# Kernel tuning notes

Measured on AMD Instinct MI355X. Metric: run time of the kernel, lower is better.

Reference implementation:

```python
import jax, jax.numpy as jnp
import numpy as np

N, D_IN, D_OUT, E = 8192, 2048, 8192, 8


def setup_inputs() -> dict:
    key = jax.random.key(0)
    k1, k2, k3 = jax.random.split(key, 3)
    x = jax.random.normal(k1, (N, D_IN), dtype=jnp.float32)
    # packed weight layout [E, in, out] (pack() pretransposes [E,out,in] -> [E,in,out])
    weight = jax.random.normal(k2, (E, D_IN, D_OUT), dtype=jnp.float32) * (1.0 / np.sqrt(D_IN))
    indices = jax.random.randint(k3, (N,), 0, E, dtype=jnp.int32)
    return {"x": x, "weight": weight, "indices": indices}


def reference(x, weight, indices):
    # gather_mm: out[n] = x[n] @ weight[indices[n]]  -> [N, D_OUT]
    # Avoid materializing weight[indices] ([N, in, out]); instead loop over the
    # small fixed expert count, masking tokens routed to each expert.
    n_experts = weight.shape[0]
    out = jnp.zeros((x.shape[0], weight.shape[-1]), dtype=x.dtype)
    for e in range(n_experts):
        mask = (indices == e)[:, None]
        xe = jnp.where(mask, x, 0)          # zero out tokens not routed to e
        out = out + xe @ weight[e]           # [N, in] @ [in, out]
    return out
```

## Files before the change

### kernel.cpp

```cpp
#include <hip/hip_runtime.h>
#include <hip/hip_bf16.h>
#include <stdint.h>

#define N_TOK 8192
#define D_IN  2048
#define D_OUT 8192
#define NEXP  8
#define KST   32
#define NT2   40
#define NS2   32
#define AIMG  32768
#define X_OFF2 65536
#define X_BYTES2 ((long)NT2 * KST * AIMG)
#define W_OFF2 (X_OFF2 + X_BYTES2)
#define W_BYTES2 ((long)NEXP * NS2 * KST * AIMG)
#define WS_NEED2 ((size_t)(W_OFF2 + W_BYTES2))


typedef float  f32x4  __attribute__((ext_vector_type(4)));
typedef __bf16 bf16x8 __attribute__((ext_vector_type(8)));

__global__ void SwitchLinear_setup_kernel(const int* __restrict__ idx,
                                          int* __restrict__ ws) {
    __shared__ int cnt[NEXP], cur[NEXP];
    int t = threadIdx.x;
    if (t < NEXP) cnt[t] = 0;
    __syncthreads();
    for (int i = t; i < N_TOK; i += 256) atomicAdd(&cnt[idx[i]], 1);
    __syncthreads();
    if (t == 0) {
        int o = 0, nt = 0, nt1 = 0;
        for (int e = 0; e < NEXP; ++e) {
            cur[e] = o;
            int c = cnt[e];
            for (int r = 0; r < c; r += 256) {
                ws[8 + nt]   = e;
                ws[96 + nt]  = o + r;
                ws[192 + nt] = (c - r < 256) ? (c - r) : 256;
                ++nt;
            }
            for (int r = 0; r < c; r += 128) {
                ws[256 + nt1] = e;
                ws[328 + nt1] = o + r;
                ws[400 + nt1] = (c - r < 128) ? (c - r) : 128;
                ++nt1;
            }
            o += c;
        }
        ws[0] = nt;
        ws[4] = nt1;
    }
    __syncthreads();
    for (int i = t; i < N_TOK; i += 256) {
        int p = atomicAdd(&cur[idx[i]], 1);
        ws[512 + p] = i;
    }
}


__global__ __launch_bounds__(256) void SwitchLinear_convx_kernel(
    const float* __restrict__ x, const int* __restrict__ ws,
    char* __restrict__ wsb) {
    const int tile = blockIdx.x, kst = blockIdx.y;
    if (tile >= ws[0]) return;
    const int rs = ws[96 + tile], rows = ws[192 + tile];
    char* img = wsb + X_OFF2 + (long)(tile * KST + kst) * AIMG;
    const int t = threadIdx.x;
#pragma unroll
    for (int i = 0; i < 8; ++i) {
        int u = t + i * 256;
        int R = u >> 3, kc8 = u & 7;
        int rl = rs + (R < rows ? R : rows - 1);
        int token = ws[512 + rl];
        const float* src = x + (long)token * D_IN + kst * 64 + kc8 * 8;
        f32x4 v0 = *(const f32x4*)src;
        f32x4 v1 = *(const f32x4*)(src + 4);
        union { __bf16 hh[8]; uint4 u4; } c;
        c.hh[0] = (__bf16)v0[0]; c.hh[1] = (__bf16)v0[1];
        c.hh[2] = (__bf16)v0[2]; c.hh[3] = (__bf16)v0[3];
        c.hh[4] = (__bf16)v1[0]; c.hh[5] = (__bf16)v1[1];
        c.hh[6] = (__bf16)v1[2]; c.hh[7] = (__bf16)v1[3];
        int slot = (((R & 1) << 2) | (kc8 & 3)) ^ ((R >> 1) & 7);
        *(uint4*)(img + (kc8 >> 2) * 16384 + ((R >> 1) << 7) + (slot << 4)) = c.u4;
    }
}

__global__ __launch_bounds__(256) void SwitchLinear_convw_kernel(
    const float* __restrict__ w, char* __restrict__ wsb) {
    const int img = blockIdx.x;
    const int kst = img & 31, s = (img >> 5) & 63, e = img >> 11;
    const int y = s >> 1, hh = s & 1;
    __shared__ float tl[64 * 129];
    const float* src = w + (long)e * D_IN * D_OUT + (long)(kst * 64) * D_OUT +
                       y * 256 + hh * 128;
    const int t = threadIdx.x;
#pragma unroll
    for (int i = 0; i < 8; ++i) {
        int u = t + i * 256;
        int row = u >> 5, ch = u & 31;
        f32x4 v = *(const f32x4*)(src + (long)row * D_OUT + ch * 4);
        float* d = &tl[row * 129 + ch * 4];
        d[0] = v[0]; d[1] = v[1]; d[2] = v[2]; d[3] = v[3];
    }
    __syncthreads();
    char* dimg = wsb + W_OFF2 + (long)((e * NS2 + y) * KST + kst) * AIMG;
#pragma unroll
    for (int i = 0; i < 4; ++i) {
        int u = t + i * 256;
        int cl = u >> 3, kc8 = u & 7;
        union { __bf16 h8[8]; uint4 u4; } c;
#pragma unroll
        for (int j = 0; j < 8; ++j) c.h8[j] = (__bf16)tl[(kc8 * 8 + j) * 129 + cl];
        int cc = hh * 128 + cl;
        int slot = (((cc & 1) << 2) | (kc8 & 3)) ^ ((cc >> 1) & 7);
        *(uint4*)(dimg + (kc8 >> 2) * 16384 + ((cc >> 1) << 7) + (slot << 4)) = c.u4;
    }
}


__global__ __launch_bounds__(512, 1) void SwitchLinear_gemm_kernel(
    const char* __restrict__ wsb, const int* __restrict__ ws,
    float* __restrict__ out) {
    const int bid = blockIdx.x;
    const int lb  = (bid & 7) * ((NT2 * NS2) / 8) + (bid >> 3);
    const int tx  = lb % NT2;
    const int y   = lb / NT2;
    if (tx >= ws[0]) return;
    const int e = ws[8 + tx], rs = ws[96 + tx], rows = ws[192 + tx];

    __shared__ __align__(16) char lds[2][2][2][16384];
    __shared__ int ord[256];

    const int t = threadIdx.x;
    if (t < 256) ord[t] = ws[512 + rs + (t < rows ? t : 0)];
    __syncthreads();

    const char* aImg = wsb + X_OFF2 + (long)(tx * KST) * AIMG;
    const char* bImg = wsb + W_OFF2 + (long)((e * NS2 + y) * KST) * AIMG;

    const int lane = t & 63;
    const int wid  = t >> 6;
    const int wr = wid >> 2, wc = wid & 3;
    const int lm = lane & 15, lk = lane >> 4;

    f32x4 acc[8][4];
#pragma unroll
    for (int i = 0; i < 8; ++i)
#pragma unroll
        for (int j = 0; j < 4; ++j) acc[i][j] = (f32x4){0.f, 0.f, 0.f, 0.f};

    bf16x8 aa[4], bb[4];

#define STG(op, ks, half, tt)                                                 \
    __builtin_amdgcn_global_load_lds(                                         \
        (const __attribute__((address_space(1))) uint32_t*)(                  \
            ((op) ? bImg : aImg) + (long)(tt) * AIMG + (ks) * 16384 +         \
            (half) * 8192 + t * 16),                                          \
        (__attribute__((address_space(3))) uint32_t*)(                        \
            &lds[(tt) & 1][op][ks][(half) * 8192 + t * 16]),                  \
        16, 0, 0)

#define SWB(r) ((((r) >> 1) << 7) + (((((((r) & 1) << 2)) | lk) ^ (((r) >> 1) & 7)) << 4))

#define LDB(p, ks)                                                            \
    do { _Pragma("unroll")                                                    \
        for (int ni = 0; ni < 4; ++ni) {                                      \
            int cc = wc * 64 + ni * 16 + lm;                                  \
            bb[ni] = *(const bf16x8*)(&lds[p][1][ks][SWB(cc)]);               \
        } } while (0)

#define LDA(p, ks, mh)                                                        \
    do { _Pragma("unroll")                                                    \
        for (int q = 0; q < 4; ++q) {                                         \
            int rr = wr * 128 + (mh) * 64 + q * 16 + lm;                      \
            aa[q] = *(const bf16x8*)(&lds[p][0][ks][SWB(rr)]);                \
        } } while (0)

#define MFMA16(mh)                                                            \
    do { _Pragma("unroll")                                                    \
        for (int q = 0; q < 4; ++q)                                           \
            _Pragma("unroll")                                                 \
            for (int ni = 0; ni < 4; ++ni)                                    \
                acc[(mh) * 4 + q][ni] = __builtin_amdgcn_mfma_f32_16x16x32_bf16( \
                    aa[q], bb[ni], acc[(mh) * 4 + q][ni], 0, 0, 0);           \
    } while (0)

#define PH(p, ks, mh, DOB, ISSUE, POST)                                       \
    do {                                                                      \
        if (DOB) LDB(p, ks);                                                  \
        LDA(p, ks, mh);                                                       \
        ISSUE;                                                                \
        __builtin_amdgcn_s_barrier();                                         \
        asm volatile("s_waitcnt lgkmcnt(0)" ::: "memory");                    \
        __builtin_amdgcn_sched_barrier(0);                                    \
        __builtin_amdgcn_s_setprio(1);                                        \
        MFMA16(mh);                                                           \
        __builtin_amdgcn_s_setprio(0);                                        \
        POST;                                                                 \
        __builtin_amdgcn_s_barrier();                                         \
    } while (0)

    STG(0, 0, 0, 0); STG(0, 0, 1, 0); STG(1, 0, 0, 0); STG(1, 0, 1, 0);
    STG(0, 1, 0, 0); STG(0, 1, 1, 0); STG(1, 1, 0, 0); STG(1, 1, 1, 0);
    asm volatile("s_waitcnt vmcnt(4)" ::: "memory");
    __builtin_amdgcn_s_barrier();

    for (int tt = 0; tt < KST - 1; ++tt) {
        const int p = tt & 1;
        const int nx = tt + 1;
        PH(p, 0, 0, 1, { STG(0, 0, 0, nx); STG(0, 0, 1, nx); }, ((void)0));
        PH(p, 0, 1, 0, { STG(1, 0, 0, nx); STG(1, 0, 1, nx); },
           asm volatile("s_waitcnt vmcnt(4)" ::: "memory"));
        PH(p, 1, 0, 1, { STG(0, 1, 0, nx); STG(0, 1, 1, nx); }, ((void)0));
        PH(p, 1, 1, 0, { STG(1, 1, 0, nx); STG(1, 1, 1, nx); },
           asm volatile("s_waitcnt vmcnt(4)" ::: "memory"));
    }
    {
        const int p = (KST - 1) & 1;
        PH(p, 0, 0, 1, ((void)0), ((void)0));
        PH(p, 0, 1, 0, ((void)0),
           asm volatile("s_waitcnt vmcnt(0)" ::: "memory"));
        PH(p, 1, 0, 1, ((void)0), ((void)0));
        PH(p, 1, 1, 0, ((void)0), ((void)0));
    }

#pragma unroll
    for (int mi = 0; mi < 8; ++mi) {
#pragma unroll
        for (int j = 0; j < 4; ++j) {
            int rl = wr * 128 + mi * 16 + lk * 4 + j;
            if (rl < rows) {
                int token = ord[rl];
                float* po = out + (long)token * D_OUT + y * 256 + wc * 64 + lm;
#pragma unroll
                for (int ni = 0; ni < 4; ++ni) po[ni * 16] = acc[mi][ni][j];
            }
        }
    }
#undef STG
#undef SWB
#undef LDB
#undef LDA
#undef MFMA16
#undef PH
}


__device__ __forceinline__ int fb_a_byte(int r, int kbyte) {
    return r * 128 + (kbyte ^ ((r & 7) << 4));
}
__device__ __forceinline__ int fb_b_byte(int n, int kbyte) {
    int slot = (n ^ (n >> 2)) & 7;
    return n * 128 + (kbyte ^ (slot << 4));
}

__global__ __launch_bounds__(256, 2) void SwitchLinear_gemm_fb_kernel(
    const float* __restrict__ x, const float* __restrict__ w,
    const int* __restrict__ ws, float* __restrict__ out) {
    const int nt = ws[4];
    const int tx = blockIdx.x;
    if (tx >= nt) return;
    const int e    = ws[256 + tx];
    const int rs   = ws[328 + tx];
    const int rows = ws[400 + tx];
    const int col0 = blockIdx.y * 128;

    __shared__ __align__(16) unsigned short As[128 * 64];
    __shared__ __align__(16) unsigned short Bs[128 * 64];
    __shared__ int ord[128];

    const int t = threadIdx.x;
    if (t < 128) {
        int r = (t < rows) ? (rs + t) : rs;
        ord[t] = ws[512 + r];
    }
    __syncthreads();

    const int kq = t & 15;
    const float* pA[8];
    int rowA[8];
#pragma unroll
    for (int i = 0; i < 8; ++i) {
        int r = (t >> 4) + 16 * i;
        rowA[i] = r;
        pA[i] = x + (long)ord[r] * D_IN + kq * 4;
    }
    const float* pB[2];
    int nB[2], kbB[2];
#pragma unroll
    for (int i = 0; i < 2; ++i) {
        int u = t + 256 * i;
        int kgf = u >> 5, q = u & 31;
        kbB[i] = kgf * 4;
        nB[i]  = q * 4;
        pB[i]  = w + (long)e * D_IN * D_OUT + (long)(kgf * 4) * D_OUT + col0 + q * 4;
    }

    const int lane = t & 63;
    const int wid  = t >> 6;
    const int wr = wid >> 1, wc = wid & 1;
    const int lm = lane & 15, lk = lane >> 4;

    f32x4 acc[4][4];
#pragma unroll
    for (int i = 0; i < 4; ++i)
#pragma unroll
        for (int j = 0; j < 4; ++j) acc[i][j] = (f32x4){0.f, 0.f, 0.f, 0.f};

    for (int k0 = 0; k0 < D_IN; k0 += 64) {
#pragma unroll
        for (int i = 0; i < 8; ++i) {
            f32x4 v = *(const f32x4*)(pA[i] + k0);
            union { __bf16 h[4]; uint2 u; } c;
            c.h[0] = (__bf16)v[0]; c.h[1] = (__bf16)v[1];
            c.h[2] = (__bf16)v[2]; c.h[3] = (__bf16)v[3];
            *(uint2*)((char*)As + fb_a_byte(rowA[i], kq * 8)) = c.u;
        }
#pragma unroll
        for (int i = 0; i < 2; ++i) {
            const float* p = pB[i] + (long)k0 * D_OUT;
            f32x4 r0 = *(const f32x4*)(p);
            f32x4 r1 = *(const f32x4*)(p + D_OUT);
            f32x4 r2 = *(const f32x4*)(p + 2 * D_OUT);
            f32x4 r3 = *(const f32x4*)(p + 3 * D_OUT);
#pragma unroll
            for (int j = 0; j < 4; ++j) {
                int n = nB[i] + j;
                union { __bf16 h[4]; uint2 u; } c;
                c.h[0] = (__bf16)r0[j]; c.h[1] = (__bf16)r1[j];
                c.h[2] = (__bf16)r2[j]; c.h[3] = (__bf16)r3[j];
                *(uint2*)((char*)Bs + fb_b_byte(n, kbB[i] * 2)) = c.u;
            }
        }
        __syncthreads();
#pragma unroll
        for (int ks = 0; ks < 2; ++ks) {
            bf16x8 a[4], b[4];
            const int kbyte = ks * 64 + lk * 16;
#pragma unroll
            for (int mi = 0; mi < 4; ++mi) {
                int r = wr * 64 + mi * 16 + lm;
                a[mi] = *(const bf16x8*)((const char*)As + fb_a_byte(r, kbyte));
            }
#pragma unroll
            for (int ni = 0; ni < 4; ++ni) {
                int n = wc * 64 + ni * 16 + lm;
                b[ni] = *(const bf16x8*)((const char*)Bs + fb_b_byte(n, kbyte));
            }
#pragma unroll
            for (int mi = 0; mi < 4; ++mi)
#pragma unroll
                for (int ni = 0; ni < 4; ++ni)
                    acc[mi][ni] = __builtin_amdgcn_mfma_f32_16x16x32_bf16(
                        a[mi], b[ni], acc[mi][ni], 0, 0, 0);
        }
        __syncthreads();
    }
#pragma unroll
    for (int mi = 0; mi < 4; ++mi) {
#pragma unroll
        for (int j = 0; j < 4; ++j) {
            int rl = wr * 64 + mi * 16 + lk * 4 + j;
            if (rl < rows) {
                int token = ord[rl];
                float* po = out + (long)token * D_OUT + col0 + wc * 64 + lm;
#pragma unroll
                for (int ni = 0; ni < 4; ++ni) po[ni * 16] = acc[mi][ni][j];
            }
        }
    }
}

extern "C" void kernel_launch(void* const* d_in, const int* in_sizes, int n_in,
                              void* d_out, int out_size, void* d_ws, size_t ws_size,
                              hipStream_t stream) {
    const float* x   = (const float*)d_in[0];
    const float* w   = (const float*)d_in[1];
    const int*   idx = (const int*)d_in[2];
    float* out = (float*)d_out;
    int*   ws  = (int*)d_ws;
    char*  wsb = (char*)d_ws;

    SwitchLinear_setup_kernel<<<1, 256, 0, stream>>>(idx, ws);
    if (ws_size >= WS_NEED2) {
        SwitchLinear_convx_kernel<<<dim3(NT2, KST), 256, 0, stream>>>(x, ws, wsb);
        SwitchLinear_convw_kernel<<<NEXP * 64 * KST, 256, 0, stream>>>(w, wsb);
        SwitchLinear_gemm_kernel<<<NT2 * NS2, 512, 0, stream>>>(wsb, ws, out);
    } else {
        dim3 grid(72, 64);
        SwitchLinear_gemm_fb_kernel<<<grid, 256, 0, stream>>>(x, w, ws, out);
    }
}
```

Measured before the change: 565.0 us.

## Triple-buffer B tiles to prefetch two stages ahead; keep token ids in registers

Splits the LDS staging into separate A (double-buffered) and B (triple-buffered) arrays so weight tiles are prefetched two K-stages ahead while activation tiles stay one ahead. The main loop now covers all stages with conditional issue and adjusted vmcnt waits. Token indices for the epilogue are loaded into registers up front, which drops the shared ord array and its initial syncthreads. The change uses more LDS (160KB) and extra registers for tok, and the vmcnt accounting with uneven in-flight load counts risks reading a tile before it arrives or stalling longer.

```diff
diff --git a/kernel.cpp b/kernel.cpp
--- a/kernel.cpp
+++ b/kernel.cpp
@@ -128,12 +128,10 @@
     if (tx >= ws[0]) return;
     const int e = ws[8 + tx], rs = ws[96 + tx], rows = ws[192 + tx];
 
-    __shared__ __align__(16) char lds[2][2][2][16384];
-    __shared__ int ord[256];
+    __shared__ __align__(16) char ldsA[2][2][16384];
+    __shared__ __align__(16) char ldsB[3][2][16384];
 
     const int t = threadIdx.x;
-    if (t < 256) ord[t] = ws[512 + rs + (t < rows ? t : 0)];
-    __syncthreads();
 
     const char* aImg = wsb + X_OFF2 + (long)(tx * KST) * AIMG;
     const char* bImg = wsb + W_OFF2 + (long)((e * NS2 + y) * KST) * AIMG;
@@ -143,6 +141,15 @@
     const int wr = wid >> 2, wc = wid & 3;
     const int lm = lane & 15, lk = lane >> 4;
 
+    int tok[8][4];
+#pragma unroll
+    for (int mi = 0; mi < 8; ++mi)
+#pragma unroll
+        for (int j = 0; j < 4; ++j) {
+            int rl = wr * 128 + mi * 16 + lk * 4 + j;
+            tok[mi][j] = ws[512 + rs + (rl < rows ? rl : 0)];
+        }
+
     f32x4 acc[8][4];
 #pragma unroll
     for (int i = 0; i < 8; ++i)
@@ -151,29 +158,36 @@
 
     bf16x8 aa[4], bb[4];
 
-#define STG(op, ks, half, tt)                                                 \
+#define STGA(ks, half, tt)                                                    \
     __builtin_amdgcn_global_load_lds(                                         \
         (const __attribute__((address_space(1))) uint32_t*)(                  \
-            ((op) ? bImg : aImg) + (long)(tt) * AIMG + (ks) * 16384 +         \
-            (half) * 8192 + t * 16),                                          \
+            aImg + (long)(tt) * AIMG + (ks) * 16384 + (half) * 8192 + t * 16),\
         (__attribute__((address_space(3))) uint32_t*)(                        \
-            &lds[(tt) & 1][op][ks][(half) * 8192 + t * 16]),                  \
+            &ldsA[(tt) & 1][ks][(half) * 8192 + t * 16]),                     \
         16, 0, 0)
 
+#define STGB(ks, half, tt)                                                    \
+    __builtin_amdgcn_global_load_lds(                                         \
+        (const __attribute__((address_space(1))) uint32_t*)(                  \
+            bImg + (long)(tt) * AIMG + (ks) * 16384 + (half) * 8192 + t * 16),\
+        (__attribute__((address_space(3))) uint32_t*)(                        \
+            &ldsB[(tt) % 3][ks][(half) * 8192 + t * 16]),                     \
+        16, 0, 0)
+
 #define SWB(r) ((((r) >> 1) << 7) + (((((((r) & 1) << 2)) | lk) ^ (((r) >> 1) & 7)) << 4))
 
-#define LDB(p, ks)                                                            \
+#define LDB(pb, ks)                                                           \
     do { _Pragma("unroll")                                                    \
         for (int ni = 0; ni < 4; ++ni) {                                      \
             int cc = wc * 64 + ni * 16 + lm;                                  \
-            bb[ni] = *(const bf16x8*)(&lds[p][1][ks][SWB(cc)]);               \
+            bb[ni] = *(const bf16x8*)(&ldsB[pb][ks][SWB(cc)]);                \
         } } while (0)
 
-#define LDA(p, ks, mh)                                                        \
+#define LDA(pa, ks, mh)                                                       \
     do { _Pragma("unroll")                                                    \
         for (int q = 0; q < 4; ++q) {                                         \
             int rr = wr * 128 + (mh) * 64 + q * 16 + lm;                      \
-            aa[q] = *(const bf16x8*)(&lds[p][0][ks][SWB(rr)]);                \
+            aa[q] = *(const bf16x8*)(&ldsA[pa][ks][SWB(rr)]);                 \
         } } while (0)
 
 #define MFMA16(mh)                                                            \
@@ -185,43 +199,45 @@
                     aa[q], bb[ni], acc[(mh) * 4 + q][ni], 0, 0, 0);           \
     } while (0)
 
-#define PH(p, ks, mh, DOB, ISSUE, POST)                                       \
+#define PH(BODY_LD, ISSUE, MH, POST)                                          \
     do {                                                                      \
-        if (DOB) LDB(p, ks);                                                  \
-        LDA(p, ks, mh);                                                       \
+        BODY_LD;                                                              \
         ISSUE;                                                                \
         __builtin_amdgcn_s_barrier();                                         \
         asm volatile("s_waitcnt lgkmcnt(0)" ::: "memory");                    \
         __builtin_amdgcn_sched_barrier(0);                                    \
         __builtin_amdgcn_s_setprio(1);                                        \
-        MFMA16(mh);                                                           \
+        MFMA16(MH);                                                           \
         __builtin_amdgcn_s_setprio(0);                                        \
         POST;                                                                 \
         __builtin_amdgcn_s_barrier();                                         \
     } while (0)
 
-    STG(0, 0, 0, 0); STG(0, 0, 1, 0); STG(1, 0, 0, 0); STG(1, 0, 1, 0);
-    STG(0, 1, 0, 0); STG(0, 1, 1, 0); STG(1, 1, 0, 0); STG(1, 1, 1, 0);
+    STGA(0, 0, 0); STGA(0, 1, 0); STGA(1, 0, 0); STGA(1, 1, 0);
+    STGB(0, 0, 0); STGB(0, 1, 0); STGB(1, 0, 0); STGB(1, 1, 0);
+    STGB(0, 0, 1); STGB(0, 1, 1); STGB(1, 0, 1); STGB(1, 1, 1);
     asm volatile("s_waitcnt vmcnt(4)" ::: "memory");
     __builtin_amdgcn_s_barrier();
 
-    for (int tt = 0; tt < KST - 1; ++tt) {
-        const int p = tt & 1;
-        const int nx = tt + 1;
-        PH(p, 0, 0, 1, { STG(0, 0, 0, nx); STG(0, 0, 1, nx); }, ((void)0));
-        PH(p, 0, 1, 0, { STG(1, 0, 0, nx); STG(1, 0, 1, nx); },
-           asm volatile("s_waitcnt vmcnt(4)" ::: "memory"));
-        PH(p, 1, 0, 1, { STG(0, 1, 0, nx); STG(0, 1, 1, nx); }, ((void)0));
-        PH(p, 1, 1, 0, { STG(1, 1, 0, nx); STG(1, 1, 1, nx); },
-           asm volatile("s_waitcnt vmcnt(4)" ::: "memory"));
-    }
-    {
-        const int p = (KST - 1) & 1;
-        PH(p, 0, 0, 1, ((void)0), ((void)0));
-        PH(p, 0, 1, 0, ((void)0),
-           asm volatile("s_waitcnt vmcnt(0)" ::: "memory"));
-        PH(p, 1, 0, 1, ((void)0), ((void)0));
-        PH(p, 1, 1, 0, ((void)0), ((void)0));
+    for (int tt = 0; tt < KST; ++tt) {
+        const int pa = tt & 1;
+        const int pb = tt % 3;
+        const int nxA = tt + 1;
+        const int nxB = tt + 2;
+        const bool iA = nxA < KST;
+        const bool iB = nxB < KST;
+        PH({ LDB(pb, 0); LDA(pa, 0, 0); },
+           { if (iA) { STGA(0, 0, nxA); STGA(0, 1, nxA); } }, 0, ((void)0));
+        PH({ LDA(pa, 0, 1); },
+           { if (iA) { STGA(1, 0, nxA); STGA(1, 1, nxA); } }, 1, ((void)0));
+        PH({ LDB(pb, 1); LDA(pa, 1, 0); },
+           { if (iB) { STGB(0, 0, nxB); STGB(0, 1, nxB); } }, 0, ((void)0));
+        PH({ LDA(pa, 1, 1); },
+           { if (iB) { STGB(1, 0, nxB); STGB(1, 1, nxB); } }, 1,
+           { if (tt < KST - 2)
+                 asm volatile("s_waitcnt vmcnt(4)" ::: "memory");
+             else if (tt == KST - 2)
+                 asm volatile("s_waitcnt vmcnt(0)" ::: "memory"); });
     }
 
 #pragma unroll
@@ -230,14 +246,14 @@
         for (int j = 0; j < 4; ++j) {
             int rl = wr * 128 + mi * 16 + lk * 4 + j;
             if (rl < rows) {
-                int token = ord[rl];
-                float* po = out + (long)token * D_OUT + y * 256 + wc * 64 + lm;
+                float* po = out + (long)tok[mi][j] * D_OUT + y * 256 + wc * 64 + lm;
 #pragma unroll
                 for (int ni = 0; ni < 4; ++ni) po[ni * 16] = acc[mi][ni][j];
             }
         }
     }
-#undef STG
+#undef STGA
+#undef STGB
 #undef SWB
 #undef LDB
 #undef LDA
```

Result: slower. 595.5 us (+5.4%).
